# Kernel tuning notes

Measured on AMD Instinct MI355X. Metric: run time of the kernel, lower is better.

## Reference

```python
import jax, jax.numpy as jnp
import numpy as np

N = 50000      # nodes
E = 600000     # edges
D = 128        # feature dim (ninput == noutput -> residual)
GN = 5000      # graph_node_size (10 graphs)
GE = 60000     # graph_edge_size
EPS_NORM = 1e-5
EPS_RED = 1e-6


def graph_norm(x, size, gamma, beta):
    # torch.split into equal graphs, per-graph mean / (std(ddof=1) + eps)
    G = x.shape[0] // size
    xr = x.reshape(G, size, -1)
    mean = xr.mean(axis=1, keepdims=True)
    std = jnp.std(xr, axis=1, keepdims=True, ddof=1)  # torch.std is unbiased
    out = ((xr - mean) / (std + EPS_NORM)).reshape(x.shape)
    return gamma * out + beta


def setup_inputs() -> dict:
    key = jax.random.key(0)
    ks = jax.random.split(key, 10)
    h = jax.random.normal(ks[0], (N, D), dtype=jnp.float32)
    e = jax.random.normal(ks[1], (E, D), dtype=jnp.float32)
    src = jax.random.randint(ks[2], (E,), 0, N, dtype=jnp.int32)
    dst = jax.random.randint(ks[3], (E,), 0, N, dtype=jnp.int32)
    snorm_n = jnp.ones((1,), jnp.float32)
    snorm_e = jnp.ones((1,), jnp.float32)
    # 5 Linear layers (fc1..fc5), stored as [in, out] so y = x @ W + b
    W = jax.random.normal(ks[4], (5, D, D), dtype=jnp.float32) * (1.0 / np.sqrt(D))
    b = jax.random.normal(ks[5], (5, D), dtype=jnp.float32) * 0.01
    gamma_h = jnp.ones((D,), jnp.float32)
    beta_h = jnp.zeros((D,), jnp.float32)
    gamma_e = jnp.ones((D,), jnp.float32)
    beta_e = jnp.zeros((D,), jnp.float32)
    return {"h": h, "e": e, "src": src, "dst": dst,
            "snorm_n": snorm_n, "snorm_e": snorm_e,
            "W": W, "b": b,
            "gamma_h": gamma_h, "beta_h": beta_h,
            "gamma_e": gamma_e, "beta_e": beta_e}


def reference(h, e, src, dst, snorm_n, snorm_e, W, b, gamma_h, beta_h, gamma_e, beta_e):
    h_in, e_in = h, e
    Ah = h @ W[0] + b[0]
    Bh = h @ W[1] + b[1]
    Ce = e @ W[2] + b[2]
    Dh = h @ W[3] + b[3]
    Eh = h @ W[4] + b[4]

    # message: e_ij = Ce + Dh[src] + Eh[dst]
    e_new = Ce + Dh[src] + Eh[dst]              # [E, D]
    sig = jax.nn.sigmoid(e_new)
    num = jax.ops.segment_sum(sig * Bh[src], dst, num_segments=N)   # [N, D]
    den = jax.ops.segment_sum(sig, dst, num_segments=N)             # [N, D]
    deg = jax.ops.segment_sum(jnp.ones((E, 1), h.dtype), dst, num_segments=N)
    h_agg = Ah + num / (den + EPS_RED)
    # DGL leaves zero-in-degree nodes untouched (keep original h)
    h_new = jnp.where(deg > 0, h_agg, h)

    h_new = h_new * snorm_n
    h_new = jax.nn.relu(graph_norm(h_new, GN, gamma_h, beta_h))
    e_out = e_new * snorm_e
    e_out = jax.nn.relu(graph_norm(e_out, GE, gamma_e, beta_e))

    # residual (ninput == noutput); dropout is identity in eval mode
    h_new = h_in + h_new
    e_out = e_in + e_out
    return (h_new, e_out)
```

## Files before the change

kernel.cpp:

```cpp
#include <hip/hip_runtime.h>
#include <math.h>

#define NNODES 50000
#define NEDGES 600000
#define DIM 128
#define GNSZ 5000
#define GESZ 60000
#define NDTOT (NNODES*DIM)
#define EPS_NORM 1e-5f
#define EPS_RED  1e-6f

union F4 { float4 v; float f[4]; };

__device__ __forceinline__ float4 ld4(const float* p){ return *(const float4*)p; }

typedef __attribute__((ext_vector_type(8))) short short8;
typedef __attribute__((ext_vector_type(4))) float f32x4;

union U8 { short8 v; unsigned short u[8]; };

__device__ __forceinline__ unsigned short f2bf(float x){
  unsigned u = __float_as_uint(x);
  u += 0x7FFFu + ((u >> 16) & 1u);
  return (unsigned short)(u >> 16);
}
__device__ __forceinline__ float bf2f(unsigned short b){
  return __uint_as_float(((unsigned)b) << 16);
}

__global__ __launch_bounds__(256) void k0_pack(
    const float* __restrict__ W,
    unsigned short* __restrict__ Whi, unsigned short* __restrict__ Wlo)
{
  int slot = blockIdx.x*256 + threadIdx.x;
  if (slot >= 10240) return;
  int lane = slot & 63;
  int ct   = (slot >> 6) & 7;
  int ks   = (slot >> 9) & 3;
  int mat  = slot >> 11;
  int g = lane >> 4;
  int col = ct*16 + (lane & 15);
  U8 ho, lo;
  #pragma unroll
  for (int e = 0; e < 8; e++){
    int k = ks*32 + g*8 + e;
    float x = W[mat*DIM*DIM + k*DIM + col];
    unsigned short hb = f2bf(x);
    ho.u[e] = hb;
    lo.u[e] = f2bf(x - bf2f(hb));
  }
  *(short8*)(Whi + (size_t)slot*8) = ho.v;
  *(short8*)(Wlo + (size_t)slot*8) = lo.v;
}

__global__ __launch_bounds__(384) void k1_node_gemm(
    const float* __restrict__ h,
    const unsigned short* __restrict__ Whi, const unsigned short* __restrict__ Wlo,
    const float* __restrict__ bias,
    float* __restrict__ Ah, float* __restrict__ Bh, float* __restrict__ Dh, float* __restrict__ Eh)
{
  const int t = threadIdx.x;
  const int w = t >> 6, l = t & 63;
  const int g = l >> 4, lr = l & 15;
  const int rbase = blockIdx.x*96 + w*16;
  const int rowA = rbase + lr;

  short8 ahi[4], alo[4];
  #pragma unroll
  for (int ks = 0; ks < 4; ks++){
    F4 q0, q1;
    if (rowA < NNODES){
      q0.v = ld4(h + (size_t)rowA*DIM + ks*32 + g*8);
      q1.v = ld4(h + (size_t)rowA*DIM + ks*32 + g*8 + 4);
    } else {
      q0.v = make_float4(0.f,0.f,0.f,0.f); q1.v = q0.v;
    }
    U8 ah, al;
    #pragma unroll
    for (int j = 0; j < 4; j++){
      unsigned short hb = f2bf(q0.f[j]);
      ah.u[j] = hb; al.u[j] = f2bf(q0.f[j] - bf2f(hb));
      hb = f2bf(q1.f[j]);
      ah.u[4+j] = hb; al.u[4+j] = f2bf(q1.f[j] - bf2f(hb));
    }
    ahi[ks] = ah.v; alo[ks] = al.v;
  }

  const int mats[4] = {0,1,3,4};
  float* outp[4] = {Ah, Bh, Dh, Eh};
  #pragma unroll 1
  for (int mi = 0; mi < 4; mi++){
    f32x4 acc[8];
    #pragma unroll
    for (int ct = 0; ct < 8; ct++) acc[ct] = (f32x4){0.f,0.f,0.f,0.f};
    #pragma unroll
    for (int ks = 0; ks < 4; ks++){
      const size_t fbase = (size_t)(mats[mi]*4 + ks)*4096 + (size_t)l*8;
      #pragma unroll
      for (int ct = 0; ct < 8; ct++){
        short8 bhi = *(const short8*)(Whi + fbase + ct*512);
        short8 blo = *(const short8*)(Wlo + fbase + ct*512);
        acc[ct] = __builtin_amdgcn_mfma_f32_16x16x32_bf16(ahi[ks], bhi, acc[ct], 0,0,0);
        acc[ct] = __builtin_amdgcn_mfma_f32_16x16x32_bf16(alo[ks], bhi, acc[ct], 0,0,0);
        acc[ct] = __builtin_amdgcn_mfma_f32_16x16x32_bf16(ahi[ks], blo, acc[ct], 0,0,0);
      }
    }
    const float* bb = bias + mats[mi]*DIM;
    #pragma unroll
    for (int r = 0; r < 4; r++){
      int row = rbase + g*4 + r;
      if (row < NNODES){
        float* op = outp[mi] + (size_t)row*DIM;
        #pragma unroll
        for (int ct = 0; ct < 8; ct++){
          int col = ct*16 + lr;
          op[col] = acc[ct][r] + bb[col];
        }
      }
    }
  }
}

__global__ void k_hist(const int* __restrict__ dst, int* __restrict__ deg)
{
  int i = blockIdx.x*256 + threadIdx.x;
  if (i < NEDGES) atomicAdd(&deg[dst[i]], 1);
}

__global__ void k_scan(const int* __restrict__ deg, int* __restrict__ off)
{
  __shared__ int tot[256];
  const int t = threadIdx.x;
  const int CH = (NNODES + 255) / 256;
  const int base = t * CH;
  int s = 0;
  for (int k = 0; k < CH; k++){
    int i = base + k;
    if (i < NNODES) s += deg[i];
  }
  tot[t] = s;
  __syncthreads();
  for (int d = 1; d < 256; d <<= 1){
    int wv = (t >= d) ? tot[t-d] : 0;
    __syncthreads();
    tot[t] += wv;
    __syncthreads();
  }
  int run = tot[t] - s;
  for (int k = 0; k < CH; k++){
    int i = base + k;
    if (i < NNODES){ off[i] = run; run += deg[i]; }
  }
  if (t == 255) off[NNODES] = run;
}

__global__ void k_scatter(const int* __restrict__ dst, const int* __restrict__ off,
                          int* __restrict__ cur, int* __restrict__ eidx)
{
  int i = blockIdx.x*256 + threadIdx.x;
  if (i < NEDGES){
    int d = dst[i];
    int p = atomicAdd(&cur[d], 1);
    eidx[off[d] + p] = i;
  }
}

__global__ __launch_bounds__(384) void k2_edge(
    const float* __restrict__ e, const int* __restrict__ src, const int* __restrict__ dst,
    const unsigned short* __restrict__ Whi, const unsigned short* __restrict__ Wlo,
    const float* __restrict__ bias,
    const float* __restrict__ Dh, const float* __restrict__ Eh,
    const float* __restrict__ snorm_e,
    float* __restrict__ e_new,
    float* __restrict__ sum_e, float* __restrict__ sumsq_e)
{
  __shared__ int ssrc[96], sdst[96];
  __shared__ float s_sum[128], s_sq[128];
  const int t = threadIdx.x;
  const int base = blockIdx.x * 96;
  if (t < 96) ssrc[t] = src[base + t];
  else if (t < 192) sdst[t-96] = dst[base + t - 96];
  else if (t < 320){ s_sum[t-192] = 0.f; s_sq[t-192] = 0.f; }
  __syncthreads();

  const int w = t >> 6, l = t & 63, g = l >> 4, lr = l & 15;
  const int rowA = base + w*16 + lr;

  f32x4 acc[8];
  #pragma unroll
  for (int ct = 0; ct < 8; ct++) acc[ct] = (f32x4){0.f,0.f,0.f,0.f};

  #pragma unroll
  for (int ks = 0; ks < 4; ks++){
    F4 q0, q1;
    q0.v = ld4(e + (size_t)rowA*DIM + ks*32 + g*8);
    q1.v = ld4(e + (size_t)rowA*DIM + ks*32 + g*8 + 4);
    U8 ah, al;
    #pragma unroll
    for (int j = 0; j < 4; j++){
      unsigned short hb = f2bf(q0.f[j]);
      ah.u[j] = hb; al.u[j] = f2bf(q0.f[j] - bf2f(hb));
      hb = f2bf(q1.f[j]);
      ah.u[4+j] = hb; al.u[4+j] = f2bf(q1.f[j] - bf2f(hb));
    }
    const size_t fbase = (size_t)(2*4 + ks)*4096 + (size_t)l*8;
    #pragma unroll
    for (int ct = 0; ct < 8; ct++){
      short8 bhi = *(const short8*)(Whi + fbase + ct*512);
      short8 blo = *(const short8*)(Wlo + fbase + ct*512);
      acc[ct] = __builtin_amdgcn_mfma_f32_16x16x32_bf16(ah.v, bhi, acc[ct], 0,0,0);
      acc[ct] = __builtin_amdgcn_mfma_f32_16x16x32_bf16(al.v, bhi, acc[ct], 0,0,0);
      acc[ct] = __builtin_amdgcn_mfma_f32_16x16x32_bf16(ah.v, blo, acc[ct], 0,0,0);
    }
  }

  const float sn = snorm_e[0];
  const float* b2 = bias + 2*DIM;
  float lsum[8], lsq[8];
  #pragma unroll
  for (int ct = 0; ct < 8; ct++){ lsum[ct] = 0.f; lsq[ct] = 0.f; }

  #pragma unroll
  for (int r = 0; r < 4; r++){
    int erow = w*16 + g*4 + r;
    int edge = base + erow;
    int sgl = ssrc[erow], dgl = sdst[erow];
    const float* dp = Dh + (size_t)sgl*DIM;
    const float* ep = Eh + (size_t)dgl*DIM;
    float* op = e_new + (size_t)edge*DIM;
    #pragma unroll
    for (int ct = 0; ct < 8; ct++){
      int col = ct*16 + lr;
      float v = acc[ct][r] + b2[col] + dp[col] + ep[col];
      op[col] = v;
      float x = v*sn;
      lsum[ct] += x; lsq[ct] += x*x;
    }
  }
  #pragma unroll
  for (int ct = 0; ct < 8; ct++){
    atomicAdd(&s_sum[ct*16 + lr], lsum[ct]);
    atomicAdd(&s_sq[ct*16 + lr],  lsq[ct]);
  }
  __syncthreads();
  if (t < 128){
    int gg = base / GESZ;
    atomicAdd(&sum_e[gg*DIM + t],   s_sum[t]);
    atomicAdd(&sumsq_e[gg*DIM + t], s_sq[t]);
  }
}

__global__ __launch_bounds__(256) void k_agg(
    const float* __restrict__ h,
    const float* __restrict__ e_new,
    const float* __restrict__ Bh,
    const int* __restrict__ src,
    const int* __restrict__ off,
    const int* __restrict__ eidx,
    const float* __restrict__ snorm_n,
    float* hbuf,
    float* __restrict__ sum_h, float* __restrict__ sumsq_h)
{
  __shared__ float s_sum[128], s_sq[128];
  const int t = threadIdx.x;
  if (t < 128){ s_sum[t]=0.f; s_sq[t]=0.f; }
  __syncthreads();
  int idx4 = blockIdx.x*256 + t;
  int node = idx4 >> 5;
  int c4 = (idx4 & 31) * 4;
  size_t offp = (size_t)node*DIM + c4;
  const int beg = off[node], end = off[node+1];
  float num[4] = {0,0,0,0}, den[4] = {0,0,0,0};
  int eid = (beg < end) ? eidx[beg] : 0;
  for (int k = beg; k < end; k++){
    int eidn = (k+1 < end) ? eidx[k+1] : 0;
    int s = src[eid];
    F4 ev; ev.v = ld4(e_new + (size_t)eid*DIM + c4);
    F4 bh; bh.v = ld4(Bh + (size_t)s*DIM + c4);
    #pragma unroll
    for (int j=0;j<4;j++){
      float sig = 1.f/(1.f + __expf(-ev.f[j]));
      num[j] += sig * bh.f[j];
      den[j] += sig;
    }
    eid = eidn;
  }
  F4 a;  a.v  = *(float4*)(hbuf + offp);
  F4 hh; hh.v = ld4(h + offp);
  const float sn = snorm_n[0];
  const bool hasdeg = (end > beg);
  F4 x;
  #pragma unroll
  for (int j=0;j<4;j++){
    float v = hasdeg ? (a.f[j] + num[j]/(den[j] + EPS_RED)) : hh.f[j];
    x.f[j] = v * sn;
  }
  *(float4*)(hbuf + offp) = x.v;
  #pragma unroll
  for (int j=0;j<4;j++){
    atomicAdd(&s_sum[c4+j], x.f[j]);
    atomicAdd(&s_sq[c4+j],  x.f[j]*x.f[j]);
  }
  __syncthreads();
  if (t < 128){
    int g = (blockIdx.x*8) / GNSZ;
    atomicAdd(&sum_h[g*DIM+t],   s_sum[t]);
    atomicAdd(&sumsq_h[g*DIM+t], s_sq[t]);
  }
}

__global__ void k4_finalize(float* __restrict__ stats)
{
  int idx = blockIdx.x*256 + threadIdx.x;
  if (idx >= 2560) return;
  int which = idx / 1280;
  int i = idx - which*1280;
  float n = which ? (float)GNSZ : (float)GESZ;
  float s  = stats[which*2560 + i];
  float sq = stats[which*2560 + 1280 + i];
  float mean = s / n;
  float var = (sq - s*s/n) / (n - 1.f);
  var = fmaxf(var, 0.f);
  float inv = 1.f / (sqrtf(var) + EPS_NORM);
  stats[5120 + which*2560 + i] = mean;
  stats[5120 + which*2560 + 1280 + i] = inv;
}

__global__ __launch_bounds__(256) void k5_norm_h(
    const float* __restrict__ h_in, const float* __restrict__ gamma, const float* __restrict__ beta,
    const float* __restrict__ stats, float* outp)
{
  int idx4 = blockIdx.x*256 + threadIdx.x;
  int node = idx4 >> 5;
  int c4 = (idx4 & 31)*4;
  int g = node / GNSZ;
  size_t off = (size_t)node*DIM + c4;
  F4 x;  x.v  = *(float4*)(outp + off);
  F4 mn; mn.v = ld4(stats + 7680 + g*DIM + c4);
  F4 iv; iv.v = ld4(stats + 8960 + g*DIM + c4);
  F4 gm; gm.v = ld4(gamma + c4);
  F4 bt; bt.v = ld4(beta + c4);
  F4 hi; hi.v = ld4(h_in + off);
  F4 o;
  #pragma unroll
  for (int j=0;j<4;j++){
    float y = gm.f[j]*((x.f[j]-mn.f[j])*iv.f[j]) + bt.f[j];
    o.f[j] = hi.f[j] + fmaxf(y, 0.f);
  }
  *(float4*)(outp + off) = o.v;
}

__global__ __launch_bounds__(256) void k5_norm_e(
    const float* __restrict__ e_in, const float* __restrict__ gamma, const float* __restrict__ beta,
    const float* __restrict__ snorm_e, const float* __restrict__ stats, float* outp)
{
  int idx4 = blockIdx.x*256 + threadIdx.x;
  int edge = idx4 >> 5;
  int c4 = (idx4 & 31)*4;
  int g = edge / GESZ;
  size_t off = (size_t)edge*DIM + c4;
  const float sn = snorm_e[0];
  F4 x;  x.v  = *(float4*)(outp + off);
  F4 mn; mn.v = ld4(stats + 5120 + g*DIM + c4);
  F4 iv; iv.v = ld4(stats + 6400 + g*DIM + c4);
  F4 gm; gm.v = ld4(gamma + c4);
  F4 bt; bt.v = ld4(beta + c4);
  F4 ei; ei.v = ld4(e_in + off);
  F4 o;
  #pragma unroll
  for (int j=0;j<4;j++){
    float xx = x.f[j]*sn;
    float y = gm.f[j]*((xx-mn.f[j])*iv.f[j]) + bt.f[j];
    o.f[j] = ei.f[j] + fmaxf(y, 0.f);
  }
  *(float4*)(outp + off) = o.v;
}

extern "C" void kernel_launch(void* const* d_in, const int* in_sizes, int n_in,
                              void* d_out, int out_size, void* d_ws, size_t ws_size,
                              hipStream_t stream)
{
  (void)in_sizes; (void)n_in; (void)out_size; (void)ws_size;
  const float* h    = (const float*)d_in[0];
  const float* e    = (const float*)d_in[1];
  const int*   src  = (const int*)d_in[2];
  const int*   dst  = (const int*)d_in[3];
  const float* snorm_n = (const float*)d_in[4];
  const float* snorm_e = (const float*)d_in[5];
  const float* W    = (const float*)d_in[6];
  const float* bias = (const float*)d_in[7];
  const float* gamma_h = (const float*)d_in[8];
  const float* beta_h  = (const float*)d_in[9];
  const float* gamma_e = (const float*)d_in[10];
  const float* beta_e  = (const float*)d_in[11];

  float* out_h = (float*)d_out;
  float* out_e = out_h + (size_t)NDTOT;
  float* ws  = (float*)d_ws;
  float* Bh  = ws;
  float* Dh  = ws + 1*(size_t)NDTOT;
  float* Eh  = ws + 2*(size_t)NDTOT;
  float* stats = ws + 3*(size_t)NDTOT;
  unsigned short* Whi = (unsigned short*)(stats + 10240);
  unsigned short* Wlo = Whi + 81920;
  int* ints  = (int*)(Wlo + 81920);
  int* ideg  = ints;
  int* icur  = ints + NNODES;
  int* ioff  = ints + 2*NNODES;
  int* ieidx = ints + 3*NNODES + 1;

  hipMemsetAsync(stats, 0, 5120*sizeof(float), stream);
  hipMemsetAsync(ints, 0, 2*(size_t)NNODES*sizeof(int), stream);

  k0_pack<<<40, 256, 0, stream>>>(W, Whi, Wlo);
  k_hist<<<(NEDGES+255)/256, 256, 0, stream>>>(dst, ideg);
  k_scan<<<1, 256, 0, stream>>>(ideg, ioff);
  k_scatter<<<(NEDGES+255)/256, 256, 0, stream>>>(dst, ioff, icur, ieidx);

  k1_node_gemm<<<521, 384, 0, stream>>>(h, Whi, Wlo, bias, out_h, Bh, Dh, Eh);
  k2_edge<<<6250, 384, 0, stream>>>(e, src, dst, Whi, Wlo, bias, Dh, Eh, snorm_e,
                                    out_e, stats, stats+1280);
  k_agg<<<6250, 256, 0, stream>>>(h, out_e, Bh, src, ioff, ieidx, snorm_n,
                                  out_h, stats+2560, stats+3840);
  k4_finalize<<<10, 256, 0, stream>>>(stats);
  k5_norm_h<<<6250, 256, 0, stream>>>(h, gamma_h, beta_h, stats, out_h);
  k5_norm_e<<<75000, 256, 0, stream>>>(e, gamma_e, beta_e, snorm_e, stats, out_e);
}
```

Measured before the change: 1.411 ms.

## Stage MFMA tiles through LDS for vectorized stores; unroll aggregation gathers by four

In the node GEMM and edge kernels, accumulator tiles are written to a padded shared-memory buffer and read back row-contiguously. Each lane can then issue float4 loads and stores for the output rows and for the Dh/Eh gathers, replacing scattered scalar 16-lane accesses. The aggregation kernel unrolls its per-node edge loop by four so several independent gathers are in flight at once. The cost is about 50KB of LDS per block, which may lower occupancy, plus extra LDS traffic and higher register pressure.

```diff
diff --git a/kernel.cpp b/kernel.cpp
--- a/kernel.cpp
+++ b/kernel.cpp
@@ -59,6 +59,7 @@
     const float* __restrict__ bias,
     float* __restrict__ Ah, float* __restrict__ Bh, float* __restrict__ Dh, float* __restrict__ Eh)
 {
+  __shared__ float tbuf[6][16][132];
   const int t = threadIdx.x;
   const int w = t >> 6, l = t & 63;
   const int g = l >> 4, lr = l & 15;
@@ -105,17 +106,28 @@
         acc[ct] = __builtin_amdgcn_mfma_f32_16x16x32_bf16(ahi[ks], blo, acc[ct], 0,0,0);
       }
     }
-    const float* bb = bias + mats[mi]*DIM;
-    #pragma unroll
-    for (int r = 0; r < 4; r++){
-      int row = rbase + g*4 + r;
+    #pragma unroll
+    for (int r = 0; r < 4; r++)
+      #pragma unroll
+      for (int ct = 0; ct < 8; ct++)
+        tbuf[w][g*4+r][ct*16+lr] = acc[ct][r];
+    F4 bb0, bb1;
+    bb0.v = ld4(bias + mats[mi]*DIM + lr*8);
+    bb1.v = ld4(bias + mats[mi]*DIM + lr*8 + 4);
+    #pragma unroll
+    for (int rb = 0; rb < 4; rb++){
+      int row16 = rb*4 + g;
+      int row = rbase + row16;
       if (row < NNODES){
-        float* op = outp[mi] + (size_t)row*DIM;
+        F4 t0, t1;
+        t0.v = *(float4*)&tbuf[w][row16][lr*8];
+        t1.v = *(float4*)&tbuf[w][row16][lr*8 + 4];
+        F4 o0, o1;
         #pragma unroll
-        for (int ct = 0; ct < 8; ct++){
-          int col = ct*16 + lr;
-          op[col] = acc[ct][r] + bb[col];
-        }
+        for (int j = 0; j < 4; j++){ o0.f[j] = t0.f[j] + bb0.f[j]; o1.f[j] = t1.f[j] + bb1.f[j]; }
+        float* op = outp[mi] + (size_t)row*DIM + lr*8;
+        *(float4*)op = o0.v;
+        *(float4*)(op + 4) = o1.v;
       }
     }
   }
@@ -174,6 +186,7 @@
     float* __restrict__ e_new,
     float* __restrict__ sum_e, float* __restrict__ sumsq_e)
 {
+  __shared__ float tbuf[6][16][132];
   __shared__ int ssrc[96], sdst[96];
   __shared__ float s_sum[128], s_sq[128];
   const int t = threadIdx.x;
@@ -214,33 +227,51 @@
     }
   }
 
+  #pragma unroll
+  for (int r = 0; r < 4; r++)
+    #pragma unroll
+    for (int ct = 0; ct < 8; ct++)
+      tbuf[w][g*4+r][ct*16+lr] = acc[ct][r];
+
   const float sn = snorm_e[0];
-  const float* b2 = bias + 2*DIM;
+  F4 bb0, bb1;
+  bb0.v = ld4(bias + 2*DIM + lr*8);
+  bb1.v = ld4(bias + 2*DIM + lr*8 + 4);
   float lsum[8], lsq[8];
   #pragma unroll
-  for (int ct = 0; ct < 8; ct++){ lsum[ct] = 0.f; lsq[ct] = 0.f; }
-
-  #pragma unroll
-  for (int r = 0; r < 4; r++){
-    int erow = w*16 + g*4 + r;
-    int edge = base + erow;
-    int sgl = ssrc[erow], dgl = sdst[erow];
-    const float* dp = Dh + (size_t)sgl*DIM;
-    const float* ep = Eh + (size_t)dgl*DIM;
-    float* op = e_new + (size_t)edge*DIM;
-    #pragma unroll
-    for (int ct = 0; ct < 8; ct++){
-      int col = ct*16 + lr;
-      float v = acc[ct][r] + b2[col] + dp[col] + ep[col];
-      op[col] = v;
-      float x = v*sn;
-      lsum[ct] += x; lsq[ct] += x*x;
-    }
-  }
-  #pragma unroll
-  for (int ct = 0; ct < 8; ct++){
-    atomicAdd(&s_sum[ct*16 + lr], lsum[ct]);
-    atomicAdd(&s_sq[ct*16 + lr],  lsq[ct]);
+  for (int j = 0; j < 8; j++){ lsum[j] = 0.f; lsq[j] = 0.f; }
+
+  #pragma unroll
+  for (int rb = 0; rb < 4; rb++){
+    int row16 = rb*4 + g;
+    int er = w*16 + row16;
+    int edge = base + er;
+    int sgl = ssrc[er], dgl = sdst[er];
+    F4 t0, t1;
+    t0.v = *(float4*)&tbuf[w][row16][lr*8];
+    t1.v = *(float4*)&tbuf[w][row16][lr*8 + 4];
+    F4 d0, d1, e0, e1;
+    d0.v = ld4(Dh + (size_t)sgl*DIM + lr*8);
+    d1.v = ld4(Dh + (size_t)sgl*DIM + lr*8 + 4);
+    e0.v = ld4(Eh + (size_t)dgl*DIM + lr*8);
+    e1.v = ld4(Eh + (size_t)dgl*DIM + lr*8 + 4);
+    F4 o0, o1;
+    #pragma unroll
+    for (int j = 0; j < 4; j++){
+      o0.f[j] = t0.f[j] + bb0.f[j] + d0.f[j] + e0.f[j];
+      o1.f[j] = t1.f[j] + bb1.f[j] + d1.f[j] + e1.f[j];
+      float x0 = o0.f[j]*sn, x1 = o1.f[j]*sn;
+      lsum[j]   += x0; lsq[j]   += x0*x0;
+      lsum[4+j] += x1; lsq[4+j] += x1*x1;
+    }
+    float* op = e_new + (size_t)edge*DIM + lr*8;
+    *(float4*)op = o0.v;
+    *(float4*)(op + 4) = o1.v;
+  }
+  #pragma unroll
+  for (int j = 0; j < 8; j++){
+    atomicAdd(&s_sum[lr*8 + j], lsum[j]);
+    atomicAdd(&s_sq[lr*8 + j],  lsq[j]);
   }
   __syncthreads();
   if (t < 128){
@@ -271,19 +302,41 @@
   size_t offp = (size_t)node*DIM + c4;
   const int beg = off[node], end = off[node+1];
   float num[4] = {0,0,0,0}, den[4] = {0,0,0,0};
-  int eid = (beg < end) ? eidx[beg] : 0;
-  for (int k = beg; k < end; k++){
-    int eidn = (k+1 < end) ? eidx[k+1] : 0;
-    int s = src[eid];
-    F4 ev; ev.v = ld4(e_new + (size_t)eid*DIM + c4);
-    F4 bh; bh.v = ld4(Bh + (size_t)s*DIM + c4);
-    #pragma unroll
-    for (int j=0;j<4;j++){
-      float sig = 1.f/(1.f + __expf(-ev.f[j]));
-      num[j] += sig * bh.f[j];
-      den[j] += sig;
-    }
-    eid = eidn;
+  int k = beg;
+  for (; k + 4 <= end; k += 4){
+    int e0 = eidx[k], e1 = eidx[k+1], e2 = eidx[k+2], e3 = eidx[k+3];
+    int s0 = src[e0], s1 = src[e1], s2 = src[e2], s3 = src[e3];
+    F4 v0, v1, v2, v3, b0, b1, b2, b3;
+    v0.v = ld4(e_new + (size_t)e0*DIM + c4);
+    v1.v = ld4(e_new + (size_t)e1*DIM + c4);
+    v2.v = ld4(e_new + (size_t)e2*DIM + c4);
+    v3.v = ld4(e_new + (size_t)e3*DIM + c4);
+    b0.v = ld4(Bh + (size_t)s0*DIM + c4);
+    b1.v = ld4(Bh + (size_t)s1*DIM + c4);
+    b2.v = ld4(Bh + (size_t)s2*DIM + c4);
+    b3.v = ld4(Bh + (size_t)s3*DIM + c4);
+    #pragma unroll
+    for (int j = 0; j < 4; j++){
+      float g0 = 1.f/(1.f + __expf(-v0.f[j]));
+      float g1 = 1.f/(1.f + __expf(-v1.f[j]));
+      float g2 = 1.f/(1.f + __expf(-v2.f[j]));
+      float g3 = 1.f/(1.f + __expf(-v3.f[j]));
+      num[j] += g0*b0.f[j] + g1*b1.f[j] + g2*b2.f[j] + g3*b3.f[j];
+      den[j] += g0 + g1 + g2 + g3;
+    }
+  }
+  for (; k < end; k++){
+    int e0 = eidx[k];
+    int s0 = src[e0];
+    F4 v0, b0;
+    v0.v = ld4(e_new + (size_t)e0*DIM + c4);
+    b0.v = ld4(Bh + (size_t)s0*DIM + c4);
+    #pragma unroll
+    for (int j = 0; j < 4; j++){
+      float g0 = 1.f/(1.f + __expf(-v0.f[j]));
+      num[j] += g0*b0.f[j];
+      den[j] += g0;
+    }
   }
   F4 a;  a.v  = *(float4*)(hbuf + offp);
   F4 hh; hh.v = ld4(h + offp);
```

Measured after the change: 1.409 ms. Within noise of the previous version (-0.1%).
